# Kernel optimization log

Hardware: AMD Instinct MI355X
Metric: run time of the kernel (lower is better)

The kernel has to match this reference:

```python
import jax, jax.numpy as jnp
import numpy as np

B, S, H, NH, L = 2, 2048, 2048, 16, 512
HD = H // NH  # head_dim = 128


def setup_inputs() -> dict:
    key = jax.random.key(0)
    k1, k2, k3, k4, k5 = jax.random.split(key, 5)
    scale = 0.02  # mimic xavier-scale init
    return {
        "q": jax.random.normal(k1, (B, S, H), dtype=jnp.float32),
        "latent_kv": jax.random.normal(k2, (B, S, L), dtype=jnp.float32),
        "Wq": jax.random.normal(k3, (H, H), dtype=jnp.float32) * scale,
        "Wkv_expand": jax.random.normal(k4, (2 * H, L), dtype=jnp.float32) * scale,
        "Wout": jax.random.normal(k5, (H, H), dtype=jnp.float32) * scale,
    }


def reference(q, latent_kv, Wq, Wkv_expand, Wout):
    b, sq, _ = q.shape
    sk = latent_kv.shape[1]
    # projections (torch Linear: x @ W.T)
    qp = q @ Wq.T                              # [B,Sq,H]
    kv = latent_kv @ Wkv_expand.T              # [B,Sk,2H]
    k, v = jnp.split(kv, 2, axis=-1)           # each [B,Sk,H]
    # split heads -> [B,NH,S,HD]
    qh = qp.reshape(b, sq, NH, HD).transpose(0, 2, 1, 3)
    kh = k.reshape(b, sk, NH, HD).transpose(0, 2, 1, 3)
    vh = v.reshape(b, sk, NH, HD).transpose(0, 2, 1, 3)
    inv_sqrt_d = 1.0 / jnp.sqrt(jnp.float32(HD))
    scores = jnp.einsum("bhqd,bhkd->bhqk", qh, kh) * inv_sqrt_d
    # causal mask (seq_q == seq_k)
    causal = jnp.tril(jnp.ones((sq, sk), dtype=bool))
    scores = jnp.where(causal, scores, jnp.finfo(scores.dtype).min)
    attn = jax.nn.softmax(scores, axis=-1)
    out = jnp.einsum("bhqk,bhkd->bhqd", attn, vh)  # [B,NH,Sq,HD]
    out = out.transpose(0, 2, 1, 3).reshape(b, sq, H)
    return out @ Wout.T
```

## Files before the change

kernel.cpp:

```cpp
#include <hip/hip_runtime.h>

#define SLEN 2048
#define NHEADS 16
#define HDIM 128

typedef __attribute__((ext_vector_type(8))) short bf16x8;
typedef __attribute__((ext_vector_type(4))) float f32x4;
typedef __attribute__((ext_vector_type(16))) float f32x16;

__device__ __forceinline__ unsigned short f2bf(float f) {
  union { float f; unsigned u; } v; v.f = f;
  unsigned r = v.u + 0x7FFFu + ((v.u >> 16) & 1u);
  return (unsigned short)(r >> 16);
}

__device__ __forceinline__ unsigned pkbf(float a, float b) {
  unsigned r;
  asm("v_cvt_pk_bf16_f32 %0, %1, %2" : "=v"(r) : "v"(a), "v"(b));
  return r;
}

__device__ __forceinline__ void gload16(const void* g, void* l) {
  __builtin_amdgcn_global_load_lds(
      (const __attribute__((address_space(1))) unsigned int*)g,
      (__attribute__((address_space(3))) unsigned int*)l, 16, 0, 0);
}

__global__ __launch_bounds__(256) void cvt_all(const float* __restrict__ q,
                                               const float* __restrict__ Wq,
                                               const float* __restrict__ lat,
                                               const float* __restrict__ Wkv,
                                               const float* __restrict__ Wout,
                                               unsigned short* __restrict__ qo,
                                               unsigned short* __restrict__ Wqo,
                                               unsigned short* __restrict__ lato,
                                               unsigned short* __restrict__ Wkvo,
                                               unsigned short* __restrict__ Wouto) {
  const int blk = blockIdx.x;
  const float* in;
  unsigned short* out;
  int base;
  if (blk < 4096)      { in = q;    out = qo;    base = 0; }
  else if (blk < 6144) { in = Wq;   out = Wqo;   base = 4096; }
  else if (blk < 7168) { in = lat;  out = lato;  base = 6144; }
  else if (blk < 8192) { in = Wkv;  out = Wkvo;  base = 7168; }
  else                 { in = Wout; out = Wouto; base = 8192; }
  const int i = (blk - base) * 256 + threadIdx.x;
  const float4* p = reinterpret_cast<const float4*>(in) + (size_t)i * 2;
  float4 a = p[0], b = p[1];
  uint4 o;
  o.x = (unsigned)f2bf(a.x) | ((unsigned)f2bf(a.y) << 16);
  o.y = (unsigned)f2bf(a.z) | ((unsigned)f2bf(a.w) << 16);
  o.z = (unsigned)f2bf(b.x) | ((unsigned)f2bf(b.y) << 16);
  o.w = (unsigned)f2bf(b.z) | ((unsigned)f2bf(b.w) << 16);
  reinterpret_cast<uint4*>(out)[i] = o;
}

template <bool OUT_F32>
__global__ __launch_bounds__(256) void gemm_bt(const unsigned short* __restrict__ A,
                                               const unsigned short* __restrict__ B,
                                               void* __restrict__ Cv,
                                               int M, int N, int K) {
  __shared__ unsigned short As[128 * 32];
  __shared__ unsigned short Bs[128 * 32];
  const int tid = threadIdx.x;
  const int lane = tid & 63, wid = tid >> 6;
  const int g = lane >> 4, q = lane & 15;
  const int nbx = N >> 7;
  const int bx = blockIdx.x % nbx, by = blockIdx.x / nbx;
  const int tM = by << 7, tN = bx << 7;
  const int wm = (wid >> 1) * 64, wn = (wid & 1) * 64;

  f32x4 acc[4][4] = {};

  const int o0 = tid * 16;
  const int r0 = o0 >> 6, c0 = (o0 & 63) >> 1;
  const int r1 = r0 + 64;
  const unsigned short* gA0 = A + (size_t)(tM + r0) * K + c0;
  const unsigned short* gA1 = A + (size_t)(tM + r1) * K + c0;
  const unsigned short* gB0 = B + (size_t)(tN + r0) * K + c0;
  const unsigned short* gB1 = B + (size_t)(tN + r1) * K + c0;
  char* lA = (char*)As;
  char* lB = (char*)Bs;
  const int wo = wid * 1024;

  for (int kt = 0; kt < K; kt += 32) {
    gload16(gA0, lA + wo);
    gload16(gA1, lA + 4096 + wo);
    gload16(gB0, lB + wo);
    gload16(gB1, lB + 4096 + wo);
    gA0 += 32; gA1 += 32; gB0 += 32; gB1 += 32;
    __syncthreads();
    bf16x8 af[4], bfr[4];
#pragma unroll
    for (int i = 0; i < 4; ++i)
      af[i] = *(const bf16x8*)&As[(wm + i * 16 + q) * 32 + g * 8];
#pragma unroll
    for (int j = 0; j < 4; ++j)
      bfr[j] = *(const bf16x8*)&Bs[(wn + j * 16 + q) * 32 + g * 8];
#pragma unroll
    for (int i = 0; i < 4; ++i)
#pragma unroll
      for (int j = 0; j < 4; ++j)
        acc[i][j] = __builtin_amdgcn_mfma_f32_16x16x32_bf16(af[i], bfr[j], acc[i][j], 0, 0, 0);
    __syncthreads();
  }

  if constexpr (OUT_F32) {
    float* C = (float*)Cv;
#pragma unroll
    for (int i = 0; i < 4; ++i)
#pragma unroll
      for (int j = 0; j < 4; ++j)
#pragma unroll
        for (int r = 0; r < 4; ++r)
          C[(size_t)(tM + wm + i * 16 + g * 4 + r) * N + (tN + wn + j * 16 + q)] =
              acc[i][j][r];
  } else {
    unsigned short* C = (unsigned short*)Cv;
#pragma unroll
    for (int i = 0; i < 4; ++i)
#pragma unroll
      for (int j = 0; j < 4; ++j)
#pragma unroll
        for (int r = 0; r < 4; ++r)
          C[(size_t)(tM + wm + i * 16 + g * 4 + r) * N + (tN + wn + j * 16 + q)] =
              f2bf(acc[i][j][r]);
  }
}

__global__ __launch_bounds__(256, 2) void mla_attn(const unsigned short* __restrict__ Q,
                                                   const unsigned short* __restrict__ K,
                                                   const unsigned short* __restrict__ VT,
                                                   unsigned short* __restrict__ AO) {
  __shared__ unsigned short Ks[2][64 * 128];
  __shared__ unsigned short Vs[2][128 * 64];

  const int tid = threadIdx.x, lane = tid & 63, w = tid >> 6;
  const int q5 = lane & 31, half = lane >> 5, q7 = lane & 7;
  const int pr = blockIdx.x >> 5, bh = blockIdx.x & 31;
  const int head = bh & 15, b = bh >> 4;

  const unsigned short* Kbase = K + (size_t)(b * 2048) * 2048 + head * 128;
  const unsigned short* Vbase = VT + (size_t)(b * 2048 + head * 128) * 2048;

  const int r0 = tid >> 4, c0 = tid & 15;
  const unsigned short* kS = Kbase + (size_t)r0 * 2048 + ((c0 ^ (r0 & 7)) << 3);
  const int d0 = tid >> 3, c3 = tid & 7;
  const unsigned short* vS = Vbase + (size_t)d0 * 2048 + ((c3 ^ (d0 & 7)) << 3);

  const float sc_f = 0.08838834764831845f;
  const int arow0 = q5 * 256;
  const int vrow0 = q5 * 128;

  for (int t2 = 0; t2 < 2; ++t2) {
    const int qt = t2 ? pr : 15 - pr;
    const int nt = 2 * qt + 2;
    const int myq = qt * 128 + w * 32 + q5;
    const unsigned short* Qrow = Q + (size_t)(b * 2048 + myq) * 2048 + head * 128;

    bf16x8 qf[8];
#pragma unroll
    for (int ks = 0; ks < 8; ++ks)
      qf[ks] = *(const bf16x8*)((const char*)Qrow + ks * 32 + half * 16);

    __syncthreads();

    {
      unsigned short* kd = &Ks[0][0] + tid * 8;
      unsigned short* vd = &Vs[0][0] + tid * 8;
#pragma unroll
      for (int s = 0; s < 4; ++s) {
        gload16(kS + (size_t)s * 16 * 2048, kd + s * 2048);
        gload16(vS + (size_t)s * 32 * 2048, vd + s * 2048);
      }
    }

    float m2 = -1e30f, l = 0.f;
    f32x16 o[4];
#pragma unroll
    for (int i = 0; i < 16; ++i) { o[0][i] = 0.f; o[1][i] = 0.f; o[2][i] = 0.f; o[3][i] = 0.f; }

    for (int kt = 0; kt < nt; ++kt) {
      const int cur = kt & 1;
      asm volatile("s_waitcnt vmcnt(0)" ::: "memory");
      __builtin_amdgcn_s_barrier();

      if (kt + 1 < nt) {
        const int kvb2 = (kt + 1) * 64;
        unsigned short* kd = &Ks[cur ^ 1][0] + tid * 8;
        unsigned short* vd = &Vs[cur ^ 1][0] + tid * 8;
        const unsigned short* ks2 = kS + (size_t)kvb2 * 2048;
        const unsigned short* vs2 = vS + kvb2;
#pragma unroll
        for (int s = 0; s < 4; ++s) {
          gload16(ks2 + (size_t)s * 16 * 2048, kd + s * 2048);
          gload16(vs2 + (size_t)s * 32 * 2048, vd + s * 2048);
        }
      }

      f32x16 st[2];
#pragma unroll
      for (int i = 0; i < 16; ++i) { st[0][i] = 0.f; st[1][i] = 0.f; }
      const char* kb = (const char*)&Ks[cur][0];
      __builtin_amdgcn_s_setprio(1);
#pragma unroll
      for (int ks = 0; ks < 8; ++ks) {
        const int cd = ks * 2 + half;
#pragma unroll
        for (int m = 0; m < 2; ++m) {
          bf16x8 kf = *(const bf16x8*)(kb + arow0 + m * 8192 + ((cd ^ q7) << 4));
          st[m] = __builtin_amdgcn_mfma_f32_32x32x16_bf16(kf, qf[ks], st[m], 0, 0, 0);
        }
      }
      __builtin_amdgcn_s_setprio(0);

      float t[32];
      const int kvb = kt * 64;
      const bool needmask = (kvb + 63 > qt * 128 + w * 32);
#pragma unroll
      for (int m = 0; m < 2; ++m)
#pragma unroll
        for (int r = 0; r < 16; ++r) {
          float s = st[m][r] * sc_f;
          if (needmask) {
            const int kvloc = m * 32 + (r & 3) + 8 * (r >> 2) + 4 * half;
            s = (kvb + kvloc <= myq) ? s : -3e38f;
          }
          t[m * 16 + r] = s;
        }
      float mx = t[0];
#pragma unroll
      for (int i = 1; i < 32; ++i) mx = fmaxf(mx, t[i]);
      mx = fmaxf(mx, __shfl_xor(mx, 32));

      if (!__all(mx <= m2 + 8.f)) {
        const float mnew = fmaxf(m2, mx);
        const float rsc = __expf(m2 - mnew);
        m2 = mnew; l *= rsc;
#pragma unroll
        for (int r = 0; r < 16; ++r) {
          const int rowv = (r & 3) + 8 * (r >> 2) + 4 * half;
          const float f = __shfl(rsc, rowv);
          o[0][r] *= f; o[1][r] *= f; o[2][r] *= f; o[3][r] *= f;
        }
      }

      float ts = 0.f;
#pragma unroll
      for (int i = 0; i < 32; ++i) { t[i] = __expf(t[i] - m2); ts += t[i]; }
      ts += __shfl_xor(ts, 32);
      l += ts;

      unsigned wpk[2][4][2];
#pragma unroll
      for (int m = 0; m < 2; ++m)
#pragma unroll
        for (int r4 = 0; r4 < 4; ++r4) {
          wpk[m][r4][0] = pkbf(t[m * 16 + r4 * 4 + 0], t[m * 16 + r4 * 4 + 1]);
          wpk[m][r4][1] = pkbf(t[m * 16 + r4 * 4 + 2], t[m * 16 + r4 * 4 + 3]);
        }

      const char* vb = (const char*)&Vs[cur][0];
#pragma unroll
      for (int ks = 0; ks < 4; ++ks) {
        const int m = ks >> 1, i = ks & 1;
        const unsigned s0 = half ? wpk[m][2 * i][0] : wpk[m][2 * i + 1][0];
        const unsigned s1 = half ? wpk[m][2 * i][1] : wpk[m][2 * i + 1][1];
        const unsigned rv0 = (unsigned)__shfl_xor((int)s0, 32);
        const unsigned rv1 = (unsigned)__shfl_xor((int)s1, 32);
        const unsigned ow0 = half ? wpk[m][2 * i + 1][0] : wpk[m][2 * i][0];
        const unsigned ow1 = half ? wpk[m][2 * i + 1][1] : wpk[m][2 * i][1];
        union { unsigned u[4]; bf16x8 v; } fr;
        fr.u[0] = half ? rv0 : ow0;
        fr.u[1] = half ? rv1 : ow1;
        fr.u[2] = half ? ow0 : rv0;
        fr.u[3] = half ? ow1 : rv1;
        const int cd = ks * 2 + half;
        __builtin_amdgcn_s_setprio(1);
#pragma unroll
        for (int nf = 0; nf < 4; ++nf) {
          bf16x8 vf = *(const bf16x8*)(vb + vrow0 + nf * 4096 + ((cd ^ q7) << 4));
          o[nf] = __builtin_amdgcn_mfma_f32_32x32x16_bf16(fr.v, vf, o[nf], 0, 0, 0);
        }
        __builtin_amdgcn_s_setprio(0);
      }
    }

    const float linv = 1.0f / l;
    unsigned short* aob = AO + (size_t)(b * 2048) * 2048 + head * 128;
#pragma unroll
    for (int r = 0; r < 16; ++r) {
      const int rowv = (r & 3) + 8 * (r >> 2) + 4 * half;
      const float f = __shfl(linv, rowv);
      const size_t qa = (size_t)(qt * 128 + w * 32 + rowv);
#pragma unroll
      for (int nf = 0; nf < 4; ++nf)
        aob[qa * 2048 + nf * 32 + q5] = f2bf(o[nf][r] * f);
    }
  }
}

extern "C" void kernel_launch(void* const* d_in, const int* in_sizes, int n_in,
                              void* d_out, int out_size, void* d_ws, size_t ws_size,
                              hipStream_t stream) {
  const float* q    = (const float*)d_in[0];
  const float* lat  = (const float*)d_in[1];
  const float* Wq   = (const float*)d_in[2];
  const float* Wkv  = (const float*)d_in[3];
  const float* Wout = (const float*)d_in[4];

  char* ws = (char*)d_ws;
  unsigned short* qbf   = (unsigned short*)(ws);
  unsigned short* aobf  = (unsigned short*)(ws);
  unsigned short* Wqbf  = (unsigned short*)(ws + 16777216);
  unsigned short* latbf = (unsigned short*)(ws + 25165824);
  unsigned short* Wkvbf = (unsigned short*)(ws + 29360128);
  unsigned short* Wobf  = (unsigned short*)(ws + 33554432);
  unsigned short* qpbf  = (unsigned short*)(ws + 41943040);
  unsigned short* Kbf   = (unsigned short*)(ws + 58720256);
  unsigned short* VTbf  = (unsigned short*)(ws + 75497472);
  unsigned short* Wvbf  = Wkvbf + (size_t)2048 * 512;

  cvt_all<<<10240, 256, 0, stream>>>(q, Wq, lat, Wkv, Wout,
                                     qbf, Wqbf, latbf, Wkvbf, Wobf);

  gemm_bt<false><<<512, 256, 0, stream>>>(qbf, Wqbf, qpbf, 4096, 2048, 2048);
  gemm_bt<false><<<512, 256, 0, stream>>>(latbf, Wkvbf, Kbf, 4096, 2048, 512);
  gemm_bt<false><<<256, 256, 0, stream>>>(Wvbf, latbf, VTbf, 2048, 2048, 512);
  gemm_bt<false><<<256, 256, 0, stream>>>(Wvbf, latbf + (size_t)2048 * 512,
                                          VTbf + (size_t)2048 * 2048, 2048, 2048, 512);
  mla_attn<<<256, 256, 0, stream>>>(qpbf, Kbf, VTbf, aobf);
  gemm_bt<true><<<512, 256, 0, stream>>>(aobf, Wobf, (float*)d_out, 4096, 2048, 2048);
}
```

Measured before the change: 263.6 us.

## Split causal attention KV range across two blocks and merge partial results

Each (batch, head, query-tile pair) is now handled by two blocks that each cover half of the causal KV tiles, doubling the attention grid. Each block writes unnormalized bf16 partial outputs plus max/sum statistics, and a new merge kernel combines them with log-sum-exp weighting into the attention output. The K shared-memory swizzle also widens from 3 to 4 bits to reduce LDS bank conflicts. The aim is to fill more CUs. The cost is an extra kernel launch, extra global traffic for partials, and rounding of partial outputs to bf16.

```diff
diff --git a/kernel.cpp b/kernel.cpp
--- a/kernel.cpp
+++ b/kernel.cpp
@@ -12,6 +12,11 @@
   union { float f; unsigned u; } v; v.f = f;
   unsigned r = v.u + 0x7FFFu + ((v.u >> 16) & 1u);
   return (unsigned short)(r >> 16);
+}
+
+__device__ __forceinline__ float bf2f(unsigned short h) {
+  union { unsigned u; float f; } v; v.u = (unsigned)h << 16;
+  return v.f;
 }
 
 __device__ __forceinline__ unsigned pkbf(float a, float b) {
@@ -132,30 +137,35 @@
 __global__ __launch_bounds__(256, 2) void mla_attn(const unsigned short* __restrict__ Q,
                                                    const unsigned short* __restrict__ K,
                                                    const unsigned short* __restrict__ VT,
-                                                   unsigned short* __restrict__ AO) {
+                                                   unsigned short* __restrict__ Opart,
+                                                   float* __restrict__ Stats) {
   __shared__ unsigned short Ks[2][64 * 128];
   __shared__ unsigned short Vs[2][128 * 64];
 
   const int tid = threadIdx.x, lane = tid & 63, w = tid >> 6;
   const int q5 = lane & 31, half = lane >> 5, q7 = lane & 7;
-  const int pr = blockIdx.x >> 5, bh = blockIdx.x & 31;
+  const int s = blockIdx.x & 1;
+  const int pr = (blockIdx.x >> 1) & 7;
+  const int bh = blockIdx.x >> 4;
   const int head = bh & 15, b = bh >> 4;
 
   const unsigned short* Kbase = K + (size_t)(b * 2048) * 2048 + head * 128;
   const unsigned short* Vbase = VT + (size_t)(b * 2048 + head * 128) * 2048;
 
   const int r0 = tid >> 4, c0 = tid & 15;
-  const unsigned short* kS = Kbase + (size_t)r0 * 2048 + ((c0 ^ (r0 & 7)) << 3);
+  const unsigned short* kS = Kbase + (size_t)r0 * 2048 + ((c0 ^ r0) << 3);
   const int d0 = tid >> 3, c3 = tid & 7;
   const unsigned short* vS = Vbase + (size_t)d0 * 2048 + ((c3 ^ (d0 & 7)) << 3);
 
   const float sc_f = 0.08838834764831845f;
   const int arow0 = q5 * 256;
   const int vrow0 = q5 * 128;
+  const int q15 = q5 & 15;
 
   for (int t2 = 0; t2 < 2; ++t2) {
     const int qt = t2 ? pr : 15 - pr;
-    const int nt = 2 * qt + 2;
+    const int kt0 = s * (qt + 1);
+    const int ktN = kt0 + qt + 1;
     const int myq = qt * 128 + w * 32 + q5;
     const unsigned short* Qrow = Q + (size_t)(b * 2048 + myq) * 2048 + head * 128;
 
@@ -167,12 +177,15 @@
     __syncthreads();
 
     {
-      unsigned short* kd = &Ks[0][0] + tid * 8;
-      unsigned short* vd = &Vs[0][0] + tid * 8;
-#pragma unroll
-      for (int s = 0; s < 4; ++s) {
-        gload16(kS + (size_t)s * 16 * 2048, kd + s * 2048);
-        gload16(vS + (size_t)s * 32 * 2048, vd + s * 2048);
+      const int kvb0 = kt0 * 64;
+      unsigned short* kd = &Ks[kt0 & 1][0] + tid * 8;
+      unsigned short* vd = &Vs[kt0 & 1][0] + tid * 8;
+      const unsigned short* ks2 = kS + (size_t)kvb0 * 2048;
+      const unsigned short* vs2 = vS + kvb0;
+#pragma unroll
+      for (int u = 0; u < 4; ++u) {
+        gload16(ks2 + (size_t)u * 16 * 2048, kd + u * 2048);
+        gload16(vs2 + (size_t)u * 32 * 2048, vd + u * 2048);
       }
     }
 
@@ -181,21 +194,21 @@
 #pragma unroll
     for (int i = 0; i < 16; ++i) { o[0][i] = 0.f; o[1][i] = 0.f; o[2][i] = 0.f; o[3][i] = 0.f; }
 
-    for (int kt = 0; kt < nt; ++kt) {
+    for (int kt = kt0; kt < ktN; ++kt) {
       const int cur = kt & 1;
       asm volatile("s_waitcnt vmcnt(0)" ::: "memory");
       __builtin_amdgcn_s_barrier();
 
-      if (kt + 1 < nt) {
+      if (kt + 1 < ktN) {
         const int kvb2 = (kt + 1) * 64;
         unsigned short* kd = &Ks[cur ^ 1][0] + tid * 8;
         unsigned short* vd = &Vs[cur ^ 1][0] + tid * 8;
         const unsigned short* ks2 = kS + (size_t)kvb2 * 2048;
         const unsigned short* vs2 = vS + kvb2;
 #pragma unroll
-        for (int s = 0; s < 4; ++s) {
-          gload16(ks2 + (size_t)s * 16 * 2048, kd + s * 2048);
-          gload16(vs2 + (size_t)s * 32 * 2048, vd + s * 2048);
+        for (int u = 0; u < 4; ++u) {
+          gload16(ks2 + (size_t)u * 16 * 2048, kd + u * 2048);
+          gload16(vs2 + (size_t)u * 32 * 2048, vd + u * 2048);
         }
       }
 
@@ -209,7 +222,7 @@
         const int cd = ks * 2 + half;
 #pragma unroll
         for (int m = 0; m < 2; ++m) {
-          bf16x8 kf = *(const bf16x8*)(kb + arow0 + m * 8192 + ((cd ^ q7) << 4));
+          bf16x8 kf = *(const bf16x8*)(kb + arow0 + m * 8192 + ((cd ^ q15) << 4));
           st[m] = __builtin_amdgcn_mfma_f32_32x32x16_bf16(kf, qf[ks], st[m], 0, 0, 0);
         }
       }
@@ -222,12 +235,12 @@
       for (int m = 0; m < 2; ++m)
 #pragma unroll
         for (int r = 0; r < 16; ++r) {
-          float s = st[m][r] * sc_f;
+          float sv = st[m][r] * sc_f;
           if (needmask) {
             const int kvloc = m * 32 + (r & 3) + 8 * (r >> 2) + 4 * half;
-            s = (kvb + kvloc <= myq) ? s : -3e38f;
+            sv = (kvb + kvloc <= myq) ? sv : -3e38f;
           }
-          t[m * 16 + r] = s;
+          t[m * 16 + r] = sv;
         }
       float mx = t[0];
 #pragma unroll
@@ -287,18 +300,50 @@
       }
     }
 
-    const float linv = 1.0f / l;
-    unsigned short* aob = AO + (size_t)(b * 2048) * 2048 + head * 128;
+    const int base_o = ((bh * 16 + qt) * 2 + s) << 14;
+    const int base_s = ((bh * 16 + qt) * 2 + s) << 8;
+    if (half == 0) {
+      Stats[base_s + (w * 32 + q5) * 2] = m2;
+      Stats[base_s + (w * 32 + q5) * 2 + 1] = l;
+    }
 #pragma unroll
     for (int r = 0; r < 16; ++r) {
       const int rowv = (r & 3) + 8 * (r >> 2) + 4 * half;
-      const float f = __shfl(linv, rowv);
-      const size_t qa = (size_t)(qt * 128 + w * 32 + rowv);
+      const int row = w * 32 + rowv;
 #pragma unroll
       for (int nf = 0; nf < 4; ++nf)
-        aob[qa * 2048 + nf * 32 + q5] = f2bf(o[nf][r] * f);
+        Opart[base_o + row * 128 + nf * 32 + q5] = f2bf(o[nf][r]);
     }
   }
+}
+
+__global__ __launch_bounds__(256) void mla_merge(const unsigned short* __restrict__ Op,
+                                                 const float* __restrict__ St,
+                                                 unsigned short* __restrict__ AO) {
+  const int idx = blockIdx.x * 256 + threadIdx.x;
+  const int rid = idx >> 4;
+  const int d0 = (idx & 15) << 3;
+  const int bhqt = rid >> 7;
+  const int row = rid & 127;
+  const int sb = bhqt << 1;
+  const float m1 = St[(sb << 8) + row * 2];
+  const float l1 = St[(sb << 8) + row * 2 + 1];
+  const float m2 = St[(sb << 8) + 256 + row * 2];
+  const float l2 = St[(sb << 8) + 256 + row * 2 + 1];
+  const float M = fmaxf(m1, m2);
+  const float w1 = __expf(m1 - M), w2 = __expf(m2 - M);
+  const float inv = 1.0f / (w1 * l1 + w2 * l2);
+  const unsigned short* p1 = Op + ((size_t)sb << 14) + row * 128 + d0;
+  bf16x8 a = *(const bf16x8*)p1;
+  bf16x8 c = *(const bf16x8*)(p1 + 16384);
+  const int bh = bhqt >> 4, qt = bhqt & 15;
+  const int head = bh & 15, b = bh >> 4;
+  unsigned short outv[8];
+#pragma unroll
+  for (int j = 0; j < 8; ++j)
+    outv[j] = f2bf((w1 * bf2f((unsigned short)a[j]) + w2 * bf2f((unsigned short)c[j])) * inv);
+  unsigned short* dst = AO + ((size_t)(b * 2048 + qt * 128 + row)) * 2048 + head * 128 + d0;
+  *(uint4*)dst = *(const uint4*)outv;
 }
 
 extern "C" void kernel_launch(void* const* d_in, const int* in_sizes, int n_in,
@@ -312,14 +357,16 @@
 
   char* ws = (char*)d_ws;
   unsigned short* qbf   = (unsigned short*)(ws);
-  unsigned short* aobf  = (unsigned short*)(ws);
+  unsigned short* Opart = (unsigned short*)(ws);
   unsigned short* Wqbf  = (unsigned short*)(ws + 16777216);
   unsigned short* latbf = (unsigned short*)(ws + 25165824);
   unsigned short* Wkvbf = (unsigned short*)(ws + 29360128);
   unsigned short* Wobf  = (unsigned short*)(ws + 33554432);
   unsigned short* qpbf  = (unsigned short*)(ws + 41943040);
   unsigned short* Kbf   = (unsigned short*)(ws + 58720256);
+  unsigned short* aobf  = (unsigned short*)(ws + 58720256);
   unsigned short* VTbf  = (unsigned short*)(ws + 75497472);
+  float*          Stats = (float*)(ws + 92274688);
   unsigned short* Wvbf  = Wkvbf + (size_t)2048 * 512;
 
   cvt_all<<<10240, 256, 0, stream>>>(q, Wq, lat, Wkv, Wout,
@@ -330,6 +377,7 @@
   gemm_bt<false><<<256, 256, 0, stream>>>(Wvbf, latbf, VTbf, 2048, 2048, 512);
   gemm_bt<false><<<256, 256, 0, stream>>>(Wvbf, latbf + (size_t)2048 * 512,
                                           VTbf + (size_t)2048 * 2048, 2048, 2048, 512);
-  mla_attn<<<256, 256, 0, stream>>>(qpbf, Kbf, VTbf, aobf);
+  mla_attn<<<512, 256, 0, stream>>>(qpbf, Kbf, VTbf, Opart, Stats);
+  mla_merge<<<4096, 256, 0, stream>>>(Opart, Stats, aobf);
   gemm_bt<true><<<512, 256, 0, stream>>>(aobf, Wobf, (float*)d_out, 4096, 2048, 2048);
 }
```

New measurement: 246.7 us. 6.4% less time.
